# Performance work log

Hardware: AMD Instinct MI355X
Metric: run time of the kernel (lower is better)

## Reference

```python
import jax, jax.numpy as jnp
import numpy as np

EPS = 1e-10
TOP_K = 2  # experts_per_token


def setup_inputs() -> dict:
    key = jax.random.key(0)
    k1, k2 = jax.random.split(key)
    dim, E = 2048, 64
    B, S = 4, 4096
    x = jax.random.normal(k1, (B * S, dim), dtype=jnp.float32)
    W = jax.random.normal(k2, (dim, E), dtype=jnp.float32) * (1.0 / np.sqrt(dim))
    b = jnp.zeros((E,), dtype=jnp.float32)
    return {"x": x, "W": W, "b": b, "batch_size": B, "seq_len": S}


def reference(x, W, b, batch_size, seq_len):
    E = W.shape[1]
    N = x.shape[0]  # batch_size * seq_len
    # gate + softmax + clamp
    scores = jax.nn.softmax(x @ W + b, axis=1)
    scores = jnp.clip(scores, EPS, 1.0 - EPS)
    # log-odds transform and rz loss over (seq, experts) per batch
    logits = jnp.log(scores / (1.0 - scores)).reshape(batch_size, seq_len, E)
    rz_loss = jnp.mean(jax.scipy.special.logsumexp(logits, axis=(1, 2)))
    # top-k experts per token
    top_scores, sel_idx = jax.lax.top_k(scores, TOP_K)  # (N, K) each
    flat_idx = sel_idx.reshape(-1)  # (N*K,)
    # histogram of assignments per expert (torch.histc with unit bins)
    num_tokens_per_expert = jax.ops.segment_sum(
        jnp.ones_like(flat_idx, dtype=jnp.float32), flat_idx, num_segments=E)
    # stable argsort groups slots by expert id, preserving token order
    perm = jnp.argsort(flat_idx, stable=True)  # (N*K,)
    top_scores_sorted = top_scores.reshape(-1)[perm]
    token_indices_experts_sorted = perm // TOP_K
    return (top_scores_sorted, token_indices_experts_sorted,
            num_tokens_per_expert, rz_loss)
```

## Files before the change

### kernel.cpp

```cpp
#include <hip/hip_runtime.h>
#include <math.h>

#define EPS_ 1e-10f
#define MARGIN 4e-3f

typedef __attribute__((ext_vector_type(8))) short sh8;
typedef __attribute__((ext_vector_type(4))) float fx4;

__device__ __forceinline__ bool betterf(float v, int i, float w, int j) {
    return (v > w) || (v == w && i < j);
}
__device__ __forceinline__ bool betterd(double v, int i, double w, int j) {
    return (v > w) || (v == w && i < j);
}
__device__ __forceinline__ unsigned short f2bf(float f) {
    unsigned u = __float_as_uint(f);
    u += 0x7fffu + ((u >> 16) & 1u);
    return (unsigned short)(u >> 16);
}
__device__ __forceinline__ float bf2f(unsigned short h) {
    return __uint_as_float(((unsigned)h) << 16);
}
__device__ __forceinline__ void cvt8(const float4 a, const float4 c, sh8& hi, sh8& lo) {
    const float v[8] = {a.x, a.y, a.z, a.w, c.x, c.y, c.z, c.w};
#pragma unroll
    for (int j = 0; j < 8; ++j) {
        const unsigned short h = f2bf(v[j]);
        hi[j] = (short)h;
        lo[j] = (short)f2bf(v[j] - bf2f(h));
    }
}
__device__ __forceinline__ void gload_lds16(const float* g, void* l) {
    __builtin_amdgcn_global_load_lds(
        (const __attribute__((address_space(1))) void*)g,
        (__attribute__((address_space(3))) void*)l, 16, 0, 0);
}

__global__ __launch_bounds__(256)
void wconv(const float* __restrict__ W, unsigned short* __restrict__ wf)
{
    const int gid = blockIdx.x * 256 + threadIdx.x;
    const int e = gid & 63, k = gid >> 6;
    const int s = k >> 5, kk = k & 31, bq = kk >> 3, j = kk & 7;
    const int t = e >> 4, n = e & 15;
    const int l = n + 16 * bq;
    const float w = W[(size_t)k * 64 + e];
    const unsigned short hi = f2bf(w);
    const unsigned short lo = f2bf(w - bf2f(hi));
    const size_t base = ((size_t)s * 4 + t) * 2;
    wf[(base + 0) * 512 + l * 8 + j] = hi;
    wf[(base + 1) * 512 + l * 8 + j] = lo;
}

#define KSPL 4
__global__ __launch_bounds__(256, 4)
void gemm_mfma(const float* __restrict__ x, const unsigned short* __restrict__ wfg,
               int dim, int N, float* __restrict__ zpart)
{
    __shared__ __align__(16) char xs[2][16384];

    const int tid  = threadIdx.x;
    const int lane = tid & 63;
    const int wv   = tid >> 6;
    const int rgs  = N / 64;
    const int ks   = blockIdx.x / rgs;
    const int rg   = blockIdx.x % rgs;
    const int r0   = rg * 64;
    const int kslice = dim / KSPL;
    const int k0   = ks * kslice;
    const int nstep = kslice / 64;

    const int m = lane & 15;
    const int q = lane >> 4;
    const int arow = wv * 16 + m;

    const int srow_lo = wv * 4 + (lane >> 4);
    const int schunk  = lane & 15;

    fx4 acc[4] = {};

    const unsigned short* wl8 = wfg + (size_t)(k0 >> 5) * 4096 + lane * 8;

#pragma unroll
    for (int r = 0; r < 4; ++r) {
        const int row = r * 16 + srow_lo;
        const int gc  = schunk ^ (row & 15);
        gload_lds16(x + (size_t)(r0 + row) * dim + k0 + gc * 4,
                    &xs[0][r * 4096 + wv * 1024]);
    }
    __syncthreads();

    for (int s = 0; s < nstep; ++s) {
        const int cb = s & 1;
        if (s + 1 < nstep) {
#pragma unroll
            for (int r = 0; r < 4; ++r) {
                const int row = r * 16 + srow_lo;
                const int gc  = schunk ^ (row & 15);
                gload_lds16(x + (size_t)(r0 + row) * dim + k0 + (s + 1) * 64 + gc * 4,
                            &xs[cb ^ 1][r * 4096 + wv * 1024]);
            }
        }
#pragma unroll
        for (int kk = 0; kk < 2; ++kk) {
            const int c0 = kk * 8 + q * 2;
            const float4 f0 = *(const float4*)&xs[cb][arow * 256 + ((c0 + 0) ^ m) * 16];
            const float4 f1 = *(const float4*)&xs[cb][arow * 256 + ((c0 + 1) ^ m) * 16];
            sh8 ah, al;
            cvt8(f0, f1, ah, al);
            const unsigned short* wk = wl8 + (size_t)(s * 2 + kk) * 4096;
#pragma unroll
            for (int te = 0; te < 4; ++te) {
                const sh8 bh = __builtin_bit_cast(sh8, *(const int4*)(wk + (te * 2 + 0) * 512));
                const sh8 bl = __builtin_bit_cast(sh8, *(const int4*)(wk + (te * 2 + 1) * 512));
                acc[te] = __builtin_amdgcn_mfma_f32_16x16x32_bf16(ah, bh, acc[te], 0, 0, 0);
                acc[te] = __builtin_amdgcn_mfma_f32_16x16x32_bf16(ah, bl, acc[te], 0, 0, 0);
                acc[te] = __builtin_amdgcn_mfma_f32_16x16x32_bf16(al, bh, acc[te], 0, 0, 0);
            }
        }
        __syncthreads();
    }

    const int n = lane & 15;
    const int g = lane >> 4;
    float* zp = zpart + ((size_t)ks * N + r0 + wv * 16) * 64;
#pragma unroll
    for (int te = 0; te < 4; ++te)
#pragma unroll
        for (int i = 0; i < 4; ++i)
            zp[(g * 4 + i) * 64 + te * 16 + n] = acc[te][i];
}

__global__ __launch_bounds__(256)
void merge_epi(const float* __restrict__ zpart, const float* __restrict__ b,
               int N, float* __restrict__ ts, int* __restrict__ sel,
               float* __restrict__ rzrow,
               int* __restrict__ nflags, int* __restrict__ flaglist)
{
    const int lane = threadIdx.x & 63;
    const int wv   = threadIdx.x >> 6;
    const int e = lane;
    const float be = b[e];

    for (int rr = 0; rr < 4; ++rr) {
        const int row = blockIdx.x * 16 + wv * 4 + rr;
        float z = be;
#pragma unroll
        for (int ks = 0; ks < KSPL; ++ks)
            z += zpart[((size_t)ks * N + row) * 64 + e];

        float v1 = z, v2 = -3.4e38f;
        int i1 = e, i2 = 1 << 30;
#pragma unroll
        for (int mm = 1; mm < 64; mm <<= 1) {
            const float wva = __shfl_xor(v1, mm, 64); const int j1 = __shfl_xor(i1, mm, 64);
            const float wvb = __shfl_xor(v2, mm, 64); const int j2 = __shfl_xor(i2, mm, 64);
            if (betterf(wva, j1, v1, i1)) {
                float nv2; int ni2;
                if (betterf(v1, i1, wvb, j2)) { nv2 = v1; ni2 = i1; }
                else                          { nv2 = wvb; ni2 = j2; }
                v1 = wva; i1 = j1; v2 = nv2; i2 = ni2;
            } else if (betterf(wva, j1, v2, i2)) { v2 = wva; i2 = j1; }
        }

        float m3 = (e == i1 || e == i2) ? -3.4e38f : z;
#pragma unroll
        for (int mm = 1; mm < 64; mm <<= 1) m3 = fmaxf(m3, __shfl_xor(m3, mm, 64));

        const float ex = expf(z - v1);
        float ssum = ex;
#pragma unroll
        for (int mm = 1; mm < 64; mm <<= 1) ssum += __shfl_xor(ssum, mm, 64);
        const float inv = 1.0f / ssum;

        float sc = fminf(fmaxf(ex * inv, EPS_), 1.0f - EPS_);
        float srz = sc / (1.0f - sc);
#pragma unroll
        for (int mm = 1; mm < 64; mm <<= 1) srz += __shfl_xor(srz, mm, 64);

        if (e == 0) {
            const float s1 = fminf(fmaxf(inv, EPS_), 1.0f - EPS_);
            const float s2 = fminf(fmaxf(expf(v2 - v1) * inv, EPS_), 1.0f - EPS_);
            ts[row * 2 + 0] = s1;
            ts[row * 2 + 1] = s2;
            sel[row * 2 + 0] = i1;
            sel[row * 2 + 1] = i2;
            rzrow[row] = srz;
            if ((v1 - v2) < MARGIN || (v2 - m3) < MARGIN) {
                const int slot = atomicAdd(nflags, 1);
                flaglist[slot] = row;
            }
        }
    }
}

__global__ __launch_bounds__(1024)
void fixup(const float* __restrict__ x, const float* __restrict__ W,
           const float* __restrict__ b, int dim,
           const int* __restrict__ nflags, const int* __restrict__ flaglist,
           float* __restrict__ ts, int* __restrict__ sel)
{
    __shared__ double red[1024];
    const int tid = threadIdx.x;
    const int e = tid & 63;
    const int q = tid >> 6;
    const int nf = *nflags;
    const int slice = dim >> 4;

    for (int f = blockIdx.x; f < nf; f += gridDim.x) {
        const int row = flaglist[f];
        const float* xr = x + (size_t)row * dim;
        const int k0 = q * slice;
        double a0 = 0.0, a1 = 0.0, a2 = 0.0, a3 = 0.0;
        for (int k = k0; k < k0 + slice; k += 4) {
            a0 = fma((double)xr[k + 0], (double)W[(size_t)(k + 0) * 64 + e], a0);
            a1 = fma((double)xr[k + 1], (double)W[(size_t)(k + 1) * 64 + e], a1);
            a2 = fma((double)xr[k + 2], (double)W[(size_t)(k + 2) * 64 + e], a2);
            a3 = fma((double)xr[k + 3], (double)W[(size_t)(k + 3) * 64 + e], a3);
        }
        red[tid] = (a0 + a1) + (a2 + a3);
        __syncthreads();
        for (int st = 512; st >= 64; st >>= 1) {
            if (tid < st) red[tid] += red[tid + st];
            __syncthreads();
        }
        if (tid < 64) {
            const double z = red[tid] + (double)b[e];
            double v1 = z, v2 = -1e300;
            int i1 = e, i2 = 1 << 30;
#pragma unroll
            for (int mm = 1; mm < 64; mm <<= 1) {
                const double w1 = __shfl_xor(v1, mm, 64); const int j1 = __shfl_xor(i1, mm, 64);
                const double w2 = __shfl_xor(v2, mm, 64); const int j2 = __shfl_xor(i2, mm, 64);
                if (betterd(w1, j1, v1, i1)) {
                    double nv2; int ni2;
                    if (betterd(v1, i1, w2, j2)) { nv2 = v1; ni2 = i1; }
                    else                         { nv2 = w2; ni2 = j2; }
                    v1 = w1; i1 = j1; v2 = nv2; i2 = ni2;
                } else if (betterd(w1, j1, v2, i2)) { v2 = w1; i2 = j1; }
            }
            float sl = expf((float)(z - v1));
            float ssum = sl;
#pragma unroll
            for (int mm = 1; mm < 64; mm <<= 1) ssum += __shfl_xor(ssum, mm, 64);
            const float inv = 1.0f / ssum;
            if (e == 0) {
                const float s1 = fminf(fmaxf(inv, EPS_), 1.0f - EPS_);
                const float s2 = fminf(fmaxf(expf((float)(v2 - v1)) * inv, EPS_), 1.0f - EPS_);
                ts[row * 2 + 0] = s1;
                ts[row * 2 + 1] = s2;
                sel[row * 2 + 0] = i1;
                sel[row * 2 + 1] = i2;
            }
        }
        __syncthreads();
    }
}

__global__ void hist_chunks(const int* __restrict__ sel, int nchunks,
                            int* __restrict__ hist, int* __restrict__ cnt2)
{
    __shared__ int cnt[64];
    const int lane = threadIdx.x;
    const int c = blockIdx.x;
    cnt[lane] = 0;
    __syncthreads();
    const int ex = sel[c * 64 + lane];
    atomicAdd(&cnt[ex], 1);
    __syncthreads();
    cnt2[(size_t)lane * nchunks + c] = cnt[lane];
    if (cnt[lane]) atomicAdd(&hist[lane], cnt[lane]);
}

__global__ void rz_batch(const float* __restrict__ rzrow,
                         const int* __restrict__ bs_p, const int* __restrict__ sl_p,
                         double* __restrict__ bsum)
{
    __shared__ double red[256];
    const int nb = bs_p[0];
    const int seq = sl_p[0];
    for (int bb = blockIdx.x; bb < nb; bb += gridDim.x) {
        double s = 0.0;
        for (int i = threadIdx.x; i < seq; i += 256)
            s += (double)rzrow[(size_t)bb * seq + i];
        red[threadIdx.x] = s;
        __syncthreads();
        for (int st = 128; st > 0; st >>= 1) {
            if (threadIdx.x < st) red[threadIdx.x] += red[threadIdx.x + st];
            __syncthreads();
        }
        if (threadIdx.x == 0) bsum[bb] = red[0];
        __syncthreads();
    }
}

__global__ void combine(const int* __restrict__ hist,
                        int* __restrict__ estart,
                        const double* __restrict__ bsum,
                        const int* __restrict__ bs_p,
                        float* __restrict__ out_cnt, float* __restrict__ out_rz)
{
    const int e = threadIdx.x;
    const int c0 = hist[e];
    int incl = c0;
#pragma unroll
    for (int mm = 1; mm < 64; mm <<= 1) {
        const int w = __shfl_up(incl, mm, 64);
        if (e >= mm) incl += w;
    }
    estart[e] = incl - c0;
    out_cnt[e] = (float)c0;
    if (e == 0) {
        const int nb = bs_p[0];
        double a = 0.0;
        for (int i = 0; i < nb; ++i) a += log(bsum[i]);
        out_rz[0] = (float)(a / nb);
    }
}

__global__ __launch_bounds__(1024)
void chunk_scan(const int* __restrict__ cnt2, const int* __restrict__ estart,
                int nchunks, int* __restrict__ cbase)
{
    __shared__ int sc[1024];
    const int e = blockIdx.x;
    const int t = threadIdx.x;
    const int v = (t < nchunks) ? cnt2[(size_t)e * nchunks + t] : 0;
    sc[t] = v;
    __syncthreads();
#pragma unroll
    for (int off = 1; off < 1024; off <<= 1) {
        const int add = (t >= off) ? sc[t - off] : 0;
        __syncthreads();
        sc[t] += add;
        __syncthreads();
    }
    if (t < nchunks)
        cbase[(size_t)t * 64 + e] = estart[e] + sc[t] - v;
}

__global__ void scatter(const int* __restrict__ sel, const float* __restrict__ ts,
                        const int* __restrict__ cbase,
                        float* __restrict__ out_sc, float* __restrict__ out_idx)
{
    __shared__ int shx[64];
    const int lane = threadIdx.x;
    const int c = blockIdx.x;
    const int idx = c * 64 + lane;
    const int ex = sel[idx];
    shx[lane] = ex;
    __syncthreads();
    int pre = 0;
#pragma unroll
    for (int j = 0; j < 64; ++j) pre += (int)((j < lane) && (shx[j] == ex));
    const int pos = cbase[c * 64 + ex] + pre;
    out_sc[pos]  = ts[idx];
    out_idx[pos] = (float)(idx >> 1);
}

extern "C" void kernel_launch(void* const* d_in, const int* in_sizes, int n_in,
                              void* d_out, int out_size, void* d_ws, size_t ws_size,
                              hipStream_t stream)
{
    const float* x = (const float*)d_in[0];
    const float* W = (const float*)d_in[1];
    const float* b = (const float*)d_in[2];
    const int* bs_p = (const int*)d_in[3];
    const int* sl_p = (const int*)d_in[4];

    const int E   = in_sizes[2];
    const int dim = in_sizes[1] / E;
    const int N   = in_sizes[0] / dim;
    const int total = N * 2;
    const int nchunks = total / 64;

    char* ws = (char*)d_ws;
    size_t off = 0;
    int*    hist     = (int*)(ws + off); off += 256;
    double* bsum     = (double*)(ws + off); off += 512;
    int*    nflags   = (int*)(ws + off); off += 256;
    int*    estart   = (int*)(ws + off); off += 256;
    float*  ts       = (float*)(ws + off); off += (size_t)total * 4;
    int*    sel      = (int*)(ws + off); off += (size_t)total * 4;
    int*    flaglist = (int*)(ws + off); off += (size_t)N * 4;
    float*  rzrow    = (float*)(ws + off); off += (size_t)N * 4;
    int*    cnt2     = (int*)(ws + off); off += (size_t)nchunks * 64 * 4;
    int*    cbase    = (int*)(ws + off); off += (size_t)nchunks * 64 * 4;
    unsigned short* wfg = (unsigned short*)(ws + off); off += (size_t)dim * 64 * 2 * 2;
    float*  zpart    = (float*)(ws + off); off += (size_t)KSPL * N * 64 * 4;

    float* out_sc  = (float*)d_out;
    float* out_idx = out_sc + total;
    float* out_cnt = out_idx + total;
    float* out_rz  = out_cnt + E;

    hipMemsetAsync(ws, 0, 1280, stream);

    hipLaunchKernelGGL(wconv, dim3(dim * 64 / 256), dim3(256), 0, stream, W, wfg);
    hipLaunchKernelGGL(gemm_mfma, dim3((N / 64) * KSPL), dim3(256), 0, stream,
                       x, wfg, dim, N, zpart);
    hipLaunchKernelGGL(merge_epi, dim3(N / 16), dim3(256), 0, stream,
                       zpart, b, N, ts, sel, rzrow, nflags, flaglist);
    hipLaunchKernelGGL(fixup, dim3(512), dim3(1024), 0, stream,
                       x, W, b, dim, nflags, flaglist, ts, sel);
    hipLaunchKernelGGL(hist_chunks, dim3(nchunks), dim3(64), 0, stream,
                       sel, nchunks, hist, cnt2);
    hipLaunchKernelGGL(rz_batch, dim3(64), dim3(256), 0, stream,
                       rzrow, bs_p, sl_p, bsum);
    hipLaunchKernelGGL(combine, dim3(1), dim3(64), 0, stream,
                       hist, estart, bsum, bs_p, out_cnt, out_rz);
    hipLaunchKernelGGL(chunk_scan, dim3(64), dim3(1024), 0, stream,
                       cnt2, estart, nchunks, cbase);
    hipLaunchKernelGGL(scatter, dim3(nchunks), dim3(64), 0, stream,
                       sel, ts, cbase, out_sc, out_idx);
}
```

Before: 102.8 us.

## Stage gate weights through LDS with async loads and halve the k-step

The GEMM kernel used to read the split bf16 gate weights straight from global memory inside the MFMA loop. It now copies them into a double-buffered LDS region with global_load_lds, alongside the x tile. To stay within the LDS budget, the k-step per iteration drops from 64 to 32, and the x swizzle becomes an 8-chunk XOR pattern. This cuts redundant per-wave global weight loads and overlaps them with compute, at the cost of twice as many barriers and loop iterations.

```diff
diff --git a/kernel.cpp b/kernel.cpp
--- a/kernel.cpp
+++ b/kernel.cpp
@@ -30,7 +30,7 @@
         lo[j] = (short)f2bf(v[j] - bf2f(h));
     }
 }
-__device__ __forceinline__ void gload_lds16(const float* g, void* l) {
+__device__ __forceinline__ void gload_lds16(const void* g, void* l) {
     __builtin_amdgcn_global_load_lds(
         (const __attribute__((address_space(1))) void*)g,
         (__attribute__((address_space(3))) void*)l, 16, 0, 0);
@@ -57,7 +57,8 @@
 void gemm_mfma(const float* __restrict__ x, const unsigned short* __restrict__ wfg,
                int dim, int N, float* __restrict__ zpart)
 {
-    __shared__ __align__(16) char xs[2][16384];
+    __shared__ __align__(16) char xs[2][8192];
+    __shared__ __align__(16) char wls[2][8192];
 
     const int tid  = threadIdx.x;
     const int lane = tid & 63;
@@ -68,25 +69,28 @@
     const int r0   = rg * 64;
     const int kslice = dim / KSPL;
     const int k0   = ks * kslice;
-    const int nstep = kslice / 64;
+    const int nstep = kslice / 32;
 
     const int m = lane & 15;
     const int q = lane >> 4;
     const int arow = wv * 16 + m;
-
-    const int srow_lo = wv * 4 + (lane >> 4);
-    const int schunk  = lane & 15;
+    const int mk = m & 7;
+
+    const int srow_in = lane >> 3;
+    const int sgc     = (lane & 7) ^ (srow_in & 7);
 
     fx4 acc[4] = {};
 
-    const unsigned short* wl8 = wfg + (size_t)(k0 >> 5) * 4096 + lane * 8;
-
-#pragma unroll
-    for (int r = 0; r < 4; ++r) {
-        const int row = r * 16 + srow_lo;
-        const int gc  = schunk ^ (row & 15);
-        gload_lds16(x + (size_t)(r0 + row) * dim + k0 + gc * 4,
-                    &xs[0][r * 4096 + wv * 1024]);
+    const char* wbytes = (const char*)wfg;
+    const size_t wstep0 = (size_t)(k0 >> 5) * 8192;
+
+#pragma unroll
+    for (int r = 0; r < 2; ++r) {
+        const int row = wv * 16 + r * 8 + srow_in;
+        gload_lds16(x + (size_t)(r0 + row) * dim + k0 + sgc * 4,
+                    &xs[0][(wv * 16 + r * 8) * 128]);
+        gload_lds16(wbytes + wstep0 + wv * 2048 + r * 1024 + lane * 16,
+                    &wls[0][wv * 2048 + r * 1024]);
     }
     __syncthreads();
 
@@ -94,25 +98,26 @@
         const int cb = s & 1;
         if (s + 1 < nstep) {
 #pragma unroll
-            for (int r = 0; r < 4; ++r) {
-                const int row = r * 16 + srow_lo;
-                const int gc  = schunk ^ (row & 15);
-                gload_lds16(x + (size_t)(r0 + row) * dim + k0 + (s + 1) * 64 + gc * 4,
-                            &xs[cb ^ 1][r * 4096 + wv * 1024]);
+            for (int r = 0; r < 2; ++r) {
+                const int row = wv * 16 + r * 8 + srow_in;
+                gload_lds16(x + (size_t)(r0 + row) * dim + k0 + (s + 1) * 32 + sgc * 4,
+                            &xs[cb ^ 1][(wv * 16 + r * 8) * 128]);
+                gload_lds16(wbytes + wstep0 + (size_t)(s + 1) * 8192
+                                  + wv * 2048 + r * 1024 + lane * 16,
+                            &wls[cb ^ 1][wv * 2048 + r * 1024]);
             }
         }
-#pragma unroll
-        for (int kk = 0; kk < 2; ++kk) {
-            const int c0 = kk * 8 + q * 2;
-            const float4 f0 = *(const float4*)&xs[cb][arow * 256 + ((c0 + 0) ^ m) * 16];
-            const float4 f1 = *(const float4*)&xs[cb][arow * 256 + ((c0 + 1) ^ m) * 16];
+        {
+            const float4 f0 = *(const float4*)&xs[cb][arow * 128 + ((2 * q + 0) ^ mk) * 16];
+            const float4 f1 = *(const float4*)&xs[cb][arow * 128 + ((2 * q + 1) ^ mk) * 16];
             sh8 ah, al;
             cvt8(f0, f1, ah, al);
-            const unsigned short* wk = wl8 + (size_t)(s * 2 + kk) * 4096;
 #pragma unroll
             for (int te = 0; te < 4; ++te) {
-                const sh8 bh = __builtin_bit_cast(sh8, *(const int4*)(wk + (te * 2 + 0) * 512));
-                const sh8 bl = __builtin_bit_cast(sh8, *(const int4*)(wk + (te * 2 + 1) * 512));
+                const sh8 bh = __builtin_bit_cast(sh8,
+                    *(const int4*)&wls[cb][(te * 2 + 0) * 1024 + lane * 16]);
+                const sh8 bl = __builtin_bit_cast(sh8,
+                    *(const int4*)&wls[cb][(te * 2 + 1) * 1024 + lane * 16]);
                 acc[te] = __builtin_amdgcn_mfma_f32_16x16x32_bf16(ah, bh, acc[te], 0, 0, 0);
                 acc[te] = __builtin_amdgcn_mfma_f32_16x16x32_bf16(ah, bl, acc[te], 0, 0, 0);
                 acc[te] = __builtin_amdgcn_mfma_f32_16x16x32_bf16(al, bh, acc[te], 0, 0, 0);
```

After: 95.25 us. -7.3%, faster.
